# Performance work log

Hardware: AMD Instinct MI355X
Metric: run time of the kernel (lower is better)

The kernel has to match this reference:

```python
import jax, jax.numpy as jnp
import numpy as np

DIM = 64
H = 4
POS_DIM = 4
NUM_IDS = 16
B = 2048
N = 64


def setup_inputs() -> dict:
    key = jax.random.key(0)
    ks = jax.random.split(key, 16)
    d8 = DIM // 8
    stdv = 1.0 / np.sqrt(DIM * DIM)
    inp = {
        "x": jax.random.normal(ks[0], (B, N, DIM), jnp.float32),
        "pos": jax.random.normal(ks[1], (B, N, POS_DIM), jnp.float32),
        "strength": jax.random.normal(ks[2], (512,), jnp.float32),
        "embed_id1": 3,
        # weights stored [in, out] (torch Linear weight transposed)
        "Wq": jax.random.normal(ks[3], (DIM, DIM), jnp.float32) * 0.05,
        "Wk": jax.random.normal(ks[4], (DIM, DIM), jnp.float32) * 0.05,
        "pos_W1": jax.random.normal(ks[5], (POS_DIM, POS_DIM), jnp.float32) * 0.3,
        "pos_b1": jnp.zeros((POS_DIM,), jnp.float32),
        "pos_W2": jax.random.normal(ks[6], (POS_DIM, d8), jnp.float32) * 0.3,
        "pos_b2": jnp.zeros((d8,), jnp.float32),
        "head_W": jax.random.normal(ks[7], (d8, H), jnp.float32) * 0.3,
        "head_b": jnp.zeros((H,), jnp.float32),
        "gate": jnp.ones((H,), jnp.float32),
        "embeds": jax.random.uniform(ks[8], (NUM_IDS, DIM * DIM), jnp.float32, -stdv, stdv),
        "out_W": jax.random.normal(ks[9], (DIM, DIM), jnp.float32) * 0.05,
        "out_b": jnp.zeros((DIM,), jnp.float32),
        "str_W": jax.random.normal(ks[10], (512, 64), jnp.float32) * 0.04,
        "str_b": jnp.zeros((64,), jnp.float32),
    }
    return inp


def reference(x, pos, strength, embed_id1, Wq, Wk, pos_W1, pos_b1, pos_W2, pos_b2,
              head_W, head_b, gate, embeds, out_W, out_b, str_W, str_b):
    Bb, Nn, dim = x.shape
    h = gate.shape[0]
    dh = dim // h

    # strength projection, added to dynamic-weight V
    s64 = strength @ str_W + str_b                       # [dim]
    E = embeds[embed_id1].reshape(dim, dim)              # per-sample V weight
    v = x @ E.T + s64                                    # F.linear(x, E) + strength
    v = v.reshape(Bb, Nn, h, dh).transpose(0, 2, 1, 3)   # [B,H,N,dh]

    # QK attention
    q = (x @ Wq).reshape(Bb, Nn, h, dh).transpose(0, 2, 1, 3)
    k = (x @ Wk).reshape(Bb, Nn, h, dh).transpose(0, 2, 1, 3)
    attn = jax.nn.softmax(jnp.einsum('bhqd,bhkd->bhqk', q, k) / np.sqrt(dh), axis=-1)

    # pairwise relative-position attention
    p = jax.nn.relu(pos @ pos_W1 + pos_b1) @ pos_W2 + pos_b2          # [B,N,dim//8]
    diff = p[:, :, None, :] - p[:, None, :, :]                        # [B,N,N,dim//8]
    pos_logits = jnp.einsum('bqkf,fh->bhqk', diff, head_W) + head_b[None, :, None, None]
    pos_attn = jax.nn.softmax(pos_logits, axis=-1)

    # sigmoid-gated mixing + renormalization
    g = jax.nn.sigmoid(gate)[None, :, None, None]
    attn = (1.0 - g) * attn + g * pos_attn
    attn = attn / jnp.sum(attn, axis=-1, keepdims=True)

    out = jnp.einsum('bhqk,bhkd->bhqd', attn, v)
    out = out.transpose(0, 2, 1, 3).reshape(Bb, Nn, dim)
    return out @ out_W + out_b
```

## Files before the change

kernel.cpp:

```cpp
#include <hip/hip_runtime.h>

typedef unsigned short u16;
typedef unsigned int u32;
typedef short bf8 __attribute__((ext_vector_type(8)));
typedef float f4v __attribute__((ext_vector_type(4)));
typedef float f16v __attribute__((ext_vector_type(16)));

#define STR 72

__device__ __forceinline__ u32 f2bf(float f){
    union{float f;u32 i;}c; c.f=f; u32 i=c.i;
    return (i + 0x7FFFu + ((i>>16)&1u)) >> 16;
}

__device__ __forceinline__ void stage_row16(const float* __restrict__ g, short* __restrict__ dst,
                                            int n, int c0){
    const float4* p = (const float4*)(g + n*64 + c0);
    float4 a=p[0], b=p[1], c=p[2], d=p[3];
    uint4 o0, o1;
    o0.x = f2bf(a.x)|(f2bf(a.y)<<16); o0.y = f2bf(a.z)|(f2bf(a.w)<<16);
    o0.z = f2bf(b.x)|(f2bf(b.y)<<16); o0.w = f2bf(b.z)|(f2bf(b.w)<<16);
    o1.x = f2bf(c.x)|(f2bf(c.y)<<16); o1.y = f2bf(c.z)|(f2bf(c.w)<<16);
    o1.z = f2bf(d.x)|(f2bf(d.y)<<16); o1.w = f2bf(d.z)|(f2bf(d.w)<<16);
    *(uint4*)&dst[n*STR + c0]     = o0;
    *(uint4*)&dst[n*STR + c0 + 8] = o1;
}

__device__ __forceinline__ void stage_wt(const float* __restrict__ W, short* __restrict__ dst, int t){
    const int kp = t >> 3, ng = t & 7;
    const float4* r0 = (const float4*)(W + (2*kp  )*64 + 8*ng);
    const float4* r1 = (const float4*)(W + (2*kp+1)*64 + 8*ng);
    float4 a0=r0[0], a1=r0[1], b0=r1[0], b1=r1[1];
    float lo[8]={a0.x,a0.y,a0.z,a0.w,a1.x,a1.y,a1.z,a1.w};
    float hi[8]={b0.x,b0.y,b0.z,b0.w,b1.x,b1.y,b1.z,b1.w};
    #pragma unroll
    for (int i=0;i<8;++i)
        *(u32*)&dst[(8*ng+i)*STR + 2*kp] = f2bf(lo[i]) | (f2bf(hi[i])<<16);
}

__device__ __forceinline__ void mmlin(const short* __restrict__ X, const short* __restrict__ Wt,
                                      int w, int l15, int quad, f4v c[4]){
    bf8 a0 = *(const bf8*)&X[(16*w + l15)*STR + quad*8];
    bf8 a1 = *(const bf8*)&X[(16*w + l15)*STR + 32 + quad*8];
    #pragma unroll
    for (int nt=0; nt<4; ++nt){
        bf8 b0 = *(const bf8*)&Wt[(16*nt + l15)*STR + quad*8];
        bf8 b1 = *(const bf8*)&Wt[(16*nt + l15)*STR + 32 + quad*8];
        c[nt] = __builtin_amdgcn_mfma_f32_16x16x32_bf16(a0, b0, c[nt], 0,0,0);
        c[nt] = __builtin_amdgcn_mfma_f32_16x16x32_bf16(a1, b1, c[nt], 0,0,0);
    }
}

__global__ __launch_bounds__(256, 2) void attn_mfma_kernel(
    const float* __restrict__ x, const float* __restrict__ pos, const float* __restrict__ strength,
    const int* __restrict__ embed_id,
    const float* __restrict__ Wq, const float* __restrict__ Wk,
    const float* __restrict__ pW1, const float* __restrict__ pb1,
    const float* __restrict__ pW2, const float* __restrict__ pb2,
    const float* __restrict__ hW, const float* __restrict__ hb,
    const float* __restrict__ gate, const float* __restrict__ embeds,
    const float* __restrict__ oW, const float* __restrict__ ob,
    const float* __restrict__ sW, const float* __restrict__ sb,
    float* __restrict__ out)
{
    __shared__ short B0[64*STR];
    __shared__ short B1[64*STR];
    __shared__ short B2[64*STR];
    __shared__ short B3[64*STR];
    __shared__ short VT[64*STR];
    __shared__ float t_lds[4][64];
    __shared__ float sp[4][64];
    __shared__ float s64v[64];

    const int t    = threadIdx.x;
    const int b    = blockIdx.x;
    const int lane = t & 63;
    const int w    = t >> 6;
    const int l15  = lane & 15;
    const int l31  = lane & 31;
    const int l5   = lane >> 5;
    const int quad = lane >> 4;
    const int n    = t >> 2;
    const int c0   = (t & 3) << 4;

    stage_row16(x + (size_t)b*4096, B0, n, c0);
    stage_wt(Wq, B1, t);
    stage_wt(Wk, VT, t);

    {
        const int d = t & 63, part = t >> 6;
        const float* wp = sW + part*128*64 + d;
        const float* s  = strength + part*128;
        float acc = 0.f;
        #pragma unroll 8
        for (int i = 0; i < 128; ++i) acc = fmaf(s[i], wp[i*64], acc);
        sp[part][d] = acc;
    }

    if (t < 64) {
        float pv[4], h1[4], p8[8];
        const float* gp = pos + ((size_t)b*64 + t)*4;
        #pragma unroll
        for (int i = 0; i < 4; ++i) pv[i] = gp[i];
        #pragma unroll
        for (int j = 0; j < 4; ++j){
            float a = pb1[j];
            #pragma unroll
            for (int i = 0; i < 4; ++i) a = fmaf(pv[i], pW1[i*4+j], a);
            h1[j] = fmaxf(a, 0.f);
        }
        #pragma unroll
        for (int f = 0; f < 8; ++f){
            float a = pb2[f];
            #pragma unroll
            for (int j = 0; j < 4; ++j) a = fmaf(h1[j], pW2[j*8+f], a);
            p8[f] = a;
        }
        #pragma unroll
        for (int h = 0; h < 4; ++h){
            float a = 0.f;
            #pragma unroll
            for (int f = 0; f < 8; ++f) a = fmaf(p8[f], hW[f*4+h], a);
            t_lds[h][t] = a;
        }
    }
    __syncthreads();

    if (t < 64) s64v[t] = sp[0][t] + sp[1][t] + sp[2][t] + sp[3][t] + sb[t];
    {
        f4v c[4];
        #pragma unroll
        for (int nt=0;nt<4;++nt){ c[nt][0]=0.f;c[nt][1]=0.f;c[nt][2]=0.f;c[nt][3]=0.f; }
        mmlin(B0, B1, w, l15, quad, c);
        __syncthreads();
        #pragma unroll
        for (int nt=0;nt<4;++nt)
            #pragma unroll
            for (int r=0;r<4;++r)
                B2[(16*w + quad*4 + r)*STR + 16*nt + l15] = (short)f2bf(0.25f*c[nt][r]);
    }
    __syncthreads();

    {
        f4v c[4];
        #pragma unroll
        for (int nt=0;nt<4;++nt){ c[nt][0]=0.f;c[nt][1]=0.f;c[nt][2]=0.f;c[nt][3]=0.f; }
        mmlin(B0, VT, w, l15, quad, c);
        stage_row16(embeds + (size_t)(*embed_id)*4096, B1, n, c0);
        __syncthreads();
        #pragma unroll
        for (int nt=0;nt<4;++nt)
            #pragma unroll
            for (int r=0;r<4;++r)
                B3[(16*w + quad*4 + r)*STR + 16*nt + l15] = (short)f2bf(c[nt][r]);
    }
    __syncthreads();

    {
        f4v c[4];
        #pragma unroll
        for (int nt=0;nt<4;++nt){ c[nt][0]=0.f;c[nt][1]=0.f;c[nt][2]=0.f;c[nt][3]=0.f; }
        mmlin(B0, B1, w, l15, quad, c);
        #pragma unroll
        for (int nt=0;nt<4;++nt){
            float sv = s64v[16*nt + l15];
            uint2 pk;
            pk.x = f2bf(c[nt][0]+sv) | (f2bf(c[nt][1]+sv)<<16);
            pk.y = f2bf(c[nt][2]+sv) | (f2bf(c[nt][3]+sv)<<16);
            *(uint2*)&VT[(16*nt + l15)*STR + 16*w + quad*4] = pk;
        }
    }
    __syncthreads();

    float g = 1.f/(1.f + __expf(-gate[w]));
    f16v S[2][2];
    {
        bf8 ka0 = *(const bf8*)&B3[(     l31)*STR + 16*w + 8*l5];
        bf8 ka1 = *(const bf8*)&B3[(32 + l31)*STR + 16*w + 8*l5];
        bf8 qb0 = *(const bf8*)&B2[(     l31)*STR + 16*w + 8*l5];
        bf8 qb1 = *(const bf8*)&B2[(32 + l31)*STR + 16*w + 8*l5];
        #pragma unroll
        for (int mt=0;mt<2;++mt)
            #pragma unroll
            for (int nt=0;nt<2;++nt)
                #pragma unroll
                for (int i=0;i<16;++i) S[mt][nt][i] = 0.f;
        S[0][0] = __builtin_amdgcn_mfma_f32_32x32x16_bf16(ka0, qb0, S[0][0], 0,0,0);
        S[0][1] = __builtin_amdgcn_mfma_f32_32x32x16_bf16(ka0, qb1, S[0][1], 0,0,0);
        S[1][0] = __builtin_amdgcn_mfma_f32_32x32x16_bf16(ka1, qb0, S[1][0], 0,0,0);
        S[1][1] = __builtin_amdgcn_mfma_f32_32x32x16_bf16(ka1, qb1, S[1][1], 0,0,0);
    }
    float ep[32];
    {
        #pragma unroll
        for (int mt=0;mt<2;++mt)
            #pragma unroll
            for (int rg=0;rg<4;++rg){
                float4 tv = *(const float4*)&t_lds[w][32*mt + 8*rg + 4*l5];
                ep[mt*16+rg*4+0] = -tv.x; ep[mt*16+rg*4+1] = -tv.y;
                ep[mt*16+rg*4+2] = -tv.z; ep[mt*16+rg*4+3] = -tv.w;
            }
        float mx = ep[0];
        #pragma unroll
        for (int i=1;i<32;++i) mx = fmaxf(mx, ep[i]);
        mx = fmaxf(mx, __shfl_xor(mx, 32));
        float sm = 0.f;
        #pragma unroll
        for (int i=0;i<32;++i){ ep[i] = __expf(ep[i]-mx); sm += ep[i]; }
        sm += __shfl_xor(sm, 32);
        float gi = g / sm;
        #pragma unroll
        for (int i=0;i<32;++i) ep[i] *= gi;
    }
    float inv[2];
    #pragma unroll
    for (int nt=0;nt<2;++nt){
        float m = S[0][nt][0];
        #pragma unroll
        for (int i=1;i<16;++i) m = fmaxf(m, S[0][nt][i]);
        #pragma unroll
        for (int i=0;i<16;++i) m = fmaxf(m, S[1][nt][i]);
        m = fmaxf(m, __shfl_xor(m, 32));
        float l = 0.f;
        #pragma unroll
        for (int mt=0;mt<2;++mt)
            #pragma unroll
            for (int i=0;i<16;++i){ float e = __expf(S[mt][nt][i]-m); S[mt][nt][i] = e; l += e; }
        l += __shfl_xor(l, 32);
        float c1 = (1.f - g) / l;
        float tot = 0.f;
        #pragma unroll
        for (int mt=0;mt<2;++mt)
            #pragma unroll
            for (int i=0;i<16;++i){ float a = fmaf(c1, S[mt][nt][i], ep[mt*16+i]); S[mt][nt][i] = a; tot += a; }
        tot += __shfl_xor(tot, 32);
        inv[nt] = 1.f / tot;
    }
    __syncthreads();

    short* Pb = (w==0) ? B0 : (w==1) ? B1 : (w==2) ? B2 : B3;
    #pragma unroll
    for (int nt=0;nt<2;++nt)
        #pragma unroll
        for (int mt=0;mt<2;++mt)
            #pragma unroll
            for (int rg=0;rg<4;++rg){
                float v0 = S[mt][nt][rg*4+0]*inv[nt], v1 = S[mt][nt][rg*4+1]*inv[nt];
                float v2 = S[mt][nt][rg*4+2]*inv[nt], v3 = S[mt][nt][rg*4+3]*inv[nt];
                uint2 pk;
                pk.x = f2bf(v0) | (f2bf(v1)<<16);
                pk.y = f2bf(v2) | (f2bf(v3)<<16);
                *(uint2*)&Pb[(32*nt + l31)*STR + 32*mt + 8*rg + 4*l5] = pk;
            }

    f4v o[4];
    {
        bf8 bv0 = *(const bf8*)&VT[(16*w + l15)*STR + quad*8];
        bf8 bv1 = *(const bf8*)&VT[(16*w + l15)*STR + 32 + quad*8];
        #pragma unroll
        for (int mt=0;mt<4;++mt){
            o[mt][0]=0.f;o[mt][1]=0.f;o[mt][2]=0.f;o[mt][3]=0.f;
            bf8 a0 = *(const bf8*)&Pb[(16*mt + l15)*STR + quad*8];
            bf8 a1 = *(const bf8*)&Pb[(16*mt + l15)*STR + 32 + quad*8];
            o[mt] = __builtin_amdgcn_mfma_f32_16x16x32_bf16(a0, bv0, o[mt], 0,0,0);
            o[mt] = __builtin_amdgcn_mfma_f32_16x16x32_bf16(a1, bv1, o[mt], 0,0,0);
        }
    }
    __syncthreads();

    #pragma unroll
    for (int mt=0;mt<4;++mt)
        #pragma unroll
        for (int r=0;r<4;++r)
            B3[(16*mt + quad*4 + r)*STR + 16*w + l15] = (short)f2bf(o[mt][r]);
    stage_wt(oW, B1, t);
    __syncthreads();

    {
        f4v c[4];
        #pragma unroll
        for (int nt=0;nt<4;++nt){
            float obv = ob[16*nt + l15];
            c[nt][0]=obv;c[nt][1]=obv;c[nt][2]=obv;c[nt][3]=obv;
        }
        mmlin(B3, B1, w, l15, quad, c);
        #pragma unroll
        for (int nt=0;nt<4;++nt)
            #pragma unroll
            for (int r=0;r<4;++r)
                out[((size_t)b*64 + 16*w + quad*4 + r)*64 + 16*nt + l15] = c[nt][r];
    }
}

extern "C" void kernel_launch(void* const* d_in, const int* in_sizes, int n_in,
                              void* d_out, int out_size, void* d_ws, size_t ws_size,
                              hipStream_t stream) {
    const int B = in_sizes[0] / (64 * 64);
    attn_mfma_kernel<<<B, 256, 0, stream>>>(
        (const float*)d_in[0],  (const float*)d_in[1],  (const float*)d_in[2],  (const int*)d_in[3],
        (const float*)d_in[4],  (const float*)d_in[5],  (const float*)d_in[6],  (const float*)d_in[7],
        (const float*)d_in[8],  (const float*)d_in[9],  (const float*)d_in[10], (const float*)d_in[11],
        (const float*)d_in[12], (const float*)d_in[13], (const float*)d_in[14], (const float*)d_in[15],
        (const float*)d_in[16], (const float*)d_in[17], (float*)d_out);
}
```

Baseline: 149.1 us.

## Split per-batch invariant weight prep into a pre-kernel and merge Q/K projections

Adds a pre-kernel that converts Wq, Wk, out_W and the selected embed matrix to bf16 once, computes the strength projection once, and precomputes each batch's position-attention softmax into workspace. The main kernel then copies pre-converted bf16 tiles instead of redoing the conversion and strength matvec in every block. It also issues the Q and K matmuls back to back and drops a barrier, using an extra LDS buffer (PX). The cost is a second kernel launch, more workspace traffic and more LDS per block, which may lower occupancy.

```diff
diff --git a/kernel.cpp b/kernel.cpp
--- a/kernel.cpp
+++ b/kernel.cpp
@@ -26,16 +26,12 @@
     *(uint4*)&dst[n*STR + c0 + 8] = o1;
 }
 
-__device__ __forceinline__ void stage_wt(const float* __restrict__ W, short* __restrict__ dst, int t){
-    const int kp = t >> 3, ng = t & 7;
-    const float4* r0 = (const float4*)(W + (2*kp  )*64 + 8*ng);
-    const float4* r1 = (const float4*)(W + (2*kp+1)*64 + 8*ng);
-    float4 a0=r0[0], a1=r0[1], b0=r1[0], b1=r1[1];
-    float lo[8]={a0.x,a0.y,a0.z,a0.w,a1.x,a1.y,a1.z,a1.w};
-    float hi[8]={b0.x,b0.y,b0.z,b0.w,b1.x,b1.y,b1.z,b1.w};
-    #pragma unroll
-    for (int i=0;i<8;++i)
-        *(u32*)&dst[(8*ng+i)*STR + 2*kp] = f2bf(lo[i]) | (f2bf(hi[i])<<16);
+__device__ __forceinline__ void copy8k(const u16* __restrict__ src, short* __restrict__ dst, int t){
+    const int r = t >> 2, cs = (t & 3) << 4;
+    const uint4* s = (const uint4*)(src + r*64 + cs);
+    uint4 a = s[0], b = s[1];
+    *(uint4*)&dst[r*STR + cs]     = a;
+    *(uint4*)&dst[r*STR + cs + 8] = b;
 }
 
 __device__ __forceinline__ void mmlin(const short* __restrict__ X, const short* __restrict__ Wt,
@@ -51,16 +47,111 @@
     }
 }
 
-__global__ __launch_bounds__(256, 2) void attn_mfma_kernel(
-    const float* __restrict__ x, const float* __restrict__ pos, const float* __restrict__ strength,
+__global__ __launch_bounds__(256) void pre_kernel(
+    const float* __restrict__ pos, const float* __restrict__ strength,
     const int* __restrict__ embed_id,
     const float* __restrict__ Wq, const float* __restrict__ Wk,
     const float* __restrict__ pW1, const float* __restrict__ pb1,
     const float* __restrict__ pW2, const float* __restrict__ pb2,
-    const float* __restrict__ hW, const float* __restrict__ hb,
-    const float* __restrict__ gate, const float* __restrict__ embeds,
-    const float* __restrict__ oW, const float* __restrict__ ob,
-    const float* __restrict__ sW, const float* __restrict__ sb,
+    const float* __restrict__ hW, const float* __restrict__ embeds,
+    const float* __restrict__ oW, const float* __restrict__ sW,
+    const float* __restrict__ sb,
+    float* __restrict__ ws_s64, float* __restrict__ ws_pat,
+    u16* __restrict__ ws_wq, u16* __restrict__ ws_wk,
+    u16* __restrict__ ws_ow, u16* __restrict__ ws_e, int B)
+{
+    const int blk = blockIdx.x;
+    const int t = threadIdx.x;
+
+    if (blk < B) {
+        __shared__ float t_l[4][64];
+        if (t < 64) {
+            float pv[4], h1[4], p8[8];
+            const float* gp = pos + ((size_t)blk*64 + t)*4;
+            #pragma unroll
+            for (int i = 0; i < 4; ++i) pv[i] = gp[i];
+            #pragma unroll
+            for (int j = 0; j < 4; ++j){
+                float a = pb1[j];
+                #pragma unroll
+                for (int i = 0; i < 4; ++i) a = fmaf(pv[i], pW1[i*4+j], a);
+                h1[j] = fmaxf(a, 0.f);
+            }
+            #pragma unroll
+            for (int f = 0; f < 8; ++f){
+                float a = pb2[f];
+                #pragma unroll
+                for (int j = 0; j < 4; ++j) a = fmaf(h1[j], pW2[j*8+f], a);
+                p8[f] = a;
+            }
+            #pragma unroll
+            for (int h = 0; h < 4; ++h){
+                float a = 0.f;
+                #pragma unroll
+                for (int f = 0; f < 8; ++f) a = fmaf(p8[f], hW[f*4+h], a);
+                t_l[h][t] = a;
+            }
+        }
+        __syncthreads();
+        const int h = t >> 6, k = t & 63;
+        float v0 = -t_l[h][k];
+        float m = v0;
+        #pragma unroll
+        for (int off = 32; off; off >>= 1) m = fmaxf(m, __shfl_xor(m, off));
+        float e = __expf(v0 - m);
+        float ssum = e;
+        #pragma unroll
+        for (int off = 32; off; off >>= 1) ssum += __shfl_xor(ssum, off);
+        ws_pat[((size_t)blk*4 + h)*64 + k] = e / ssum;
+        return;
+    }
+
+    const int j = blk - B;
+    if (j < 3) {
+        const float* W = (j==0) ? Wq : (j==1) ? Wk : oW;
+        u16* dst = (j==0) ? ws_wq : (j==1) ? ws_wk : ws_ow;
+        const int kp = t >> 3, ng = t & 7;
+        const float4* r0 = (const float4*)(W + (2*kp  )*64 + 8*ng);
+        const float4* r1 = (const float4*)(W + (2*kp+1)*64 + 8*ng);
+        float4 a0=r0[0], a1=r0[1], b0=r1[0], b1=r1[1];
+        float lo[8]={a0.x,a0.y,a0.z,a0.w,a1.x,a1.y,a1.z,a1.w};
+        float hi[8]={b0.x,b0.y,b0.z,b0.w,b1.x,b1.y,b1.z,b1.w};
+        #pragma unroll
+        for (int i=0;i<8;++i)
+            *(u32*)&dst[(8*ng+i)*64 + 2*kp] = f2bf(lo[i]) | (f2bf(hi[i])<<16);
+    } else {
+        __shared__ float sp[4][64];
+        {
+            const int n = t >> 2, c0 = (t & 3) << 4;
+            const float4* p = (const float4*)(embeds + (size_t)(*embed_id)*4096 + n*64 + c0);
+            float4 a=p[0], b=p[1], c=p[2], d=p[3];
+            uint4 o0, o1;
+            o0.x = f2bf(a.x)|(f2bf(a.y)<<16); o0.y = f2bf(a.z)|(f2bf(a.w)<<16);
+            o0.z = f2bf(b.x)|(f2bf(b.y)<<16); o0.w = f2bf(b.z)|(f2bf(b.w)<<16);
+            o1.x = f2bf(c.x)|(f2bf(c.y)<<16); o1.y = f2bf(c.z)|(f2bf(c.w)<<16);
+            o1.z = f2bf(d.x)|(f2bf(d.y)<<16); o1.w = f2bf(d.z)|(f2bf(d.w)<<16);
+            *(uint4*)&ws_e[n*64 + c0]     = o0;
+            *(uint4*)&ws_e[n*64 + c0 + 8] = o1;
+        }
+        {
+            const int d = t & 63, part = t >> 6;
+            const float* wp = sW + part*128*64 + d;
+            const float* s  = strength + part*128;
+            float acc = 0.f;
+            #pragma unroll 8
+            for (int i = 0; i < 128; ++i) acc = fmaf(s[i], wp[i*64], acc);
+            sp[part][d] = acc;
+        }
+        __syncthreads();
+        if (t < 64) ws_s64[t] = sp[0][t] + sp[1][t] + sp[2][t] + sp[3][t] + sb[t];
+    }
+}
+
+__global__ __launch_bounds__(256, 2) void attn_main_kernel(
+    const float* __restrict__ x, const float* __restrict__ gate, const float* __restrict__ ob,
+    const float* __restrict__ ws_s64, const float* __restrict__ ws_pat,
+    const u16* __restrict__ ws_wq, const u16* __restrict__ ws_wk,
+    const u16* __restrict__ ws_ow, const u16* __restrict__ ws_e,
     float* __restrict__ out)
 {
     __shared__ short B0[64*STR];
@@ -68,9 +159,7 @@
     __shared__ short B2[64*STR];
     __shared__ short B3[64*STR];
     __shared__ short VT[64*STR];
-    __shared__ float t_lds[4][64];
-    __shared__ float sp[4][64];
-    __shared__ float s64v[64];
+    __shared__ short PX[64*STR];
 
     const int t    = threadIdx.x;
     const int b    = blockIdx.x;
@@ -84,49 +173,49 @@
     const int c0   = (t & 3) << 4;
 
     stage_row16(x + (size_t)b*4096, B0, n, c0);
-    stage_wt(Wq, B1, t);
-    stage_wt(Wk, VT, t);
-
-    {
-        const int d = t & 63, part = t >> 6;
-        const float* wp = sW + part*128*64 + d;
-        const float* s  = strength + part*128;
-        float acc = 0.f;
-        #pragma unroll 8
-        for (int i = 0; i < 128; ++i) acc = fmaf(s[i], wp[i*64], acc);
-        sp[part][d] = acc;
-    }
-
-    if (t < 64) {
-        float pv[4], h1[4], p8[8];
-        const float* gp = pos + ((size_t)b*64 + t)*4;
-        #pragma unroll
-        for (int i = 0; i < 4; ++i) pv[i] = gp[i];
-        #pragma unroll
-        for (int j = 0; j < 4; ++j){
-            float a = pb1[j];
-            #pragma unroll
-            for (int i = 0; i < 4; ++i) a = fmaf(pv[i], pW1[i*4+j], a);
-            h1[j] = fmaxf(a, 0.f);
-        }
-        #pragma unroll
-        for (int f = 0; f < 8; ++f){
-            float a = pb2[f];
-            #pragma unroll
-            for (int j = 0; j < 4; ++j) a = fmaf(h1[j], pW2[j*8+f], a);
-            p8[f] = a;
-        }
-        #pragma unroll
-        for (int h = 0; h < 4; ++h){
-            float a = 0.f;
-            #pragma unroll
-            for (int f = 0; f < 8; ++f) a = fmaf(p8[f], hW[f*4+h], a);
-            t_lds[h][t] = a;
-        }
-    }
-    __syncthreads();
-
-    if (t < 64) s64v[t] = sp[0][t] + sp[1][t] + sp[2][t] + sp[3][t] + sb[t];
+    copy8k(ws_wq, B1, t);
+    copy8k(ws_wk, VT, t);
+
+    uint4 eA, eB, owA, owB;
+    {
+        const int r = t >> 2, cs = (t & 3) << 4;
+        const uint4* se = (const uint4*)(ws_e + r*64 + cs);
+        eA = se[0]; eB = se[1];
+        const uint4* so = (const uint4*)(ws_ow + r*64 + cs);
+        owA = so[0]; owB = so[1];
+    }
+    float svv[4];
+    #pragma unroll
+    for (int nt=0;nt<4;++nt) svv[nt] = ws_s64[16*nt + l15];
+    float g = 1.f/(1.f + __expf(-gate[w]));
+    float obv[4];
+    #pragma unroll
+    for (int nt=0;nt<4;++nt) obv[nt] = ob[16*nt + l15];
+    __syncthreads();
+
+    {
+        f4v cq[4], ck[4];
+        #pragma unroll
+        for (int nt=0;nt<4;++nt){
+            cq[nt][0]=0.f;cq[nt][1]=0.f;cq[nt][2]=0.f;cq[nt][3]=0.f;
+            ck[nt][0]=0.f;ck[nt][1]=0.f;ck[nt][2]=0.f;ck[nt][3]=0.f;
+        }
+        mmlin(B0, B1, w, l15, quad, cq);
+        mmlin(B0, VT, w, l15, quad, ck);
+        __syncthreads();
+        #pragma unroll
+        for (int nt=0;nt<4;++nt)
+            #pragma unroll
+            for (int r=0;r<4;++r){
+                B2[(16*w + quad*4 + r)*STR + 16*nt + l15] = (short)f2bf(0.25f*cq[nt][r]);
+                B3[(16*w + quad*4 + r)*STR + 16*nt + l15] = (short)f2bf(ck[nt][r]);
+            }
+        const int r = t >> 2, cs = (t & 3) << 4;
+        *(uint4*)&B1[r*STR + cs]     = eA;
+        *(uint4*)&B1[r*STR + cs + 8] = eB;
+    }
+    __syncthreads();
+
     {
         f4v c[4];
         #pragma unroll
@@ -134,45 +223,19 @@
         mmlin(B0, B1, w, l15, quad, c);
         __syncthreads();
         #pragma unroll
-        for (int nt=0;nt<4;++nt)
-            #pragma unroll
-            for (int r=0;r<4;++r)
-                B2[(16*w + quad*4 + r)*STR + 16*nt + l15] = (short)f2bf(0.25f*c[nt][r]);
-    }
-    __syncthreads();
-
-    {
-        f4v c[4];
-        #pragma unroll
-        for (int nt=0;nt<4;++nt){ c[nt][0]=0.f;c[nt][1]=0.f;c[nt][2]=0.f;c[nt][3]=0.f; }
-        mmlin(B0, VT, w, l15, quad, c);
-        stage_row16(embeds + (size_t)(*embed_id)*4096, B1, n, c0);
-        __syncthreads();
-        #pragma unroll
-        for (int nt=0;nt<4;++nt)
-            #pragma unroll
-            for (int r=0;r<4;++r)
-                B3[(16*w + quad*4 + r)*STR + 16*nt + l15] = (short)f2bf(c[nt][r]);
-    }
-    __syncthreads();
-
-    {
-        f4v c[4];
-        #pragma unroll
-        for (int nt=0;nt<4;++nt){ c[nt][0]=0.f;c[nt][1]=0.f;c[nt][2]=0.f;c[nt][3]=0.f; }
-        mmlin(B0, B1, w, l15, quad, c);
-        #pragma unroll
         for (int nt=0;nt<4;++nt){
-            float sv = s64v[16*nt + l15];
+            float sv = svv[nt];
             uint2 pk;
             pk.x = f2bf(c[nt][0]+sv) | (f2bf(c[nt][1]+sv)<<16);
             pk.y = f2bf(c[nt][2]+sv) | (f2bf(c[nt][3]+sv)<<16);
             *(uint2*)&VT[(16*nt + l15)*STR + 16*w + quad*4] = pk;
         }
-    }
-    __syncthreads();
-
-    float g = 1.f/(1.f + __expf(-gate[w]));
+        const int r = t >> 2, cs = (t & 3) << 4;
+        *(uint4*)&B1[r*STR + cs]     = owA;
+        *(uint4*)&B1[r*STR + cs + 8] = owB;
+    }
+    __syncthreads();
+
     f16v S[2][2];
     {
         bf8 ka0 = *(const bf8*)&B3[(     l31)*STR + 16*w + 8*l5];
@@ -192,25 +255,15 @@
     }
     float ep[32];
     {
+        const float* pp = ws_pat + ((size_t)b*4 + w)*64;
         #pragma unroll
         for (int mt=0;mt<2;++mt)
             #pragma unroll
             for (int rg=0;rg<4;++rg){
-                float4 tv = *(const float4*)&t_lds[w][32*mt + 8*rg + 4*l5];
-                ep[mt*16+rg*4+0] = -tv.x; ep[mt*16+rg*4+1] = -tv.y;
-                ep[mt*16+rg*4+2] = -tv.z; ep[mt*16+rg*4+3] = -tv.w;
-            }
-        float mx = ep[0];
-        #pragma unroll
-        for (int i=1;i<32;++i) mx = fmaxf(mx, ep[i]);
-        mx = fmaxf(mx, __shfl_xor(mx, 32));
-        float sm = 0.f;
-        #pragma unroll
-        for (int i=0;i<32;++i){ ep[i] = __expf(ep[i]-mx); sm += ep[i]; }
-        sm += __shfl_xor(sm, 32);
-        float gi = g / sm;
-        #pragma unroll
-        for (int i=0;i<32;++i) ep[i] *= gi;
+                float4 tv = *(const float4*)&pp[32*mt + 8*rg + 4*l5];
+                ep[mt*16+rg*4+0] = g*tv.x; ep[mt*16+rg*4+1] = g*tv.y;
+                ep[mt*16+rg*4+2] = g*tv.z; ep[mt*16+rg*4+3] = g*tv.w;
+            }
     }
     float inv[2];
     #pragma unroll
@@ -238,7 +291,7 @@
     }
     __syncthreads();
 
-    short* Pb = (w==0) ? B0 : (w==1) ? B1 : (w==2) ? B2 : B3;
+    short* Pb = (w==0) ? B0 : (w==1) ? PX : (w==2) ? B2 : B3;
     #pragma unroll
     for (int nt=0;nt<2;++nt)
         #pragma unroll
@@ -273,15 +326,13 @@
         #pragma unroll
         for (int r=0;r<4;++r)
             B3[(16*mt + quad*4 + r)*STR + 16*w + l15] = (short)f2bf(o[mt][r]);
-    stage_wt(oW, B1, t);
     __syncthreads();
 
     {
         f4v c[4];
         #pragma unroll
         for (int nt=0;nt<4;++nt){
-            float obv = ob[16*nt + l15];
-            c[nt][0]=obv;c[nt][1]=obv;c[nt][2]=obv;c[nt][3]=obv;
+            c[nt][0]=obv[nt];c[nt][1]=obv[nt];c[nt][2]=obv[nt];c[nt][3]=obv[nt];
         }
         mmlin(B3, B1, w, l15, quad, c);
         #pragma unroll
@@ -296,10 +347,24 @@
                               void* d_out, int out_size, void* d_ws, size_t ws_size,
                               hipStream_t stream) {
     const int B = in_sizes[0] / (64 * 64);
-    attn_mfma_kernel<<<B, 256, 0, stream>>>(
-        (const float*)d_in[0],  (const float*)d_in[1],  (const float*)d_in[2],  (const int*)d_in[3],
-        (const float*)d_in[4],  (const float*)d_in[5],  (const float*)d_in[6],  (const float*)d_in[7],
-        (const float*)d_in[8],  (const float*)d_in[9],  (const float*)d_in[10], (const float*)d_in[11],
-        (const float*)d_in[12], (const float*)d_in[13], (const float*)d_in[14], (const float*)d_in[15],
-        (const float*)d_in[16], (const float*)d_in[17], (float*)d_out);
-}
+
+    float* ws_s64 = (float*)d_ws;
+    float* ws_pat = ws_s64 + 64;
+    u16*   ws_wq  = (u16*)(ws_pat + (size_t)B*4*64);
+    u16*   ws_wk  = ws_wq + 4096;
+    u16*   ws_ow  = ws_wk + 4096;
+    u16*   ws_e   = ws_ow + 4096;
+
+    pre_kernel<<<B + 4, 256, 0, stream>>>(
+        (const float*)d_in[1],  (const float*)d_in[2],  (const int*)d_in[3],
+        (const float*)d_in[4],  (const float*)d_in[5],
+        (const float*)d_in[6],  (const float*)d_in[7],  (const float*)d_in[8],  (const float*)d_in[9],
+        (const float*)d_in[10], (const float*)d_in[13], (const float*)d_in[14],
+        (const float*)d_in[16], (const float*)d_in[17],
+        ws_s64, ws_pat, ws_wq, ws_wk, ws_ow, ws_e, B);
+
+    attn_main_kernel<<<B, 256, 0, stream>>>(
+        (const float*)d_in[0],  (const float*)d_in[12], (const float*)d_in[15],
+        ws_s64, ws_pat, ws_wq, ws_wk, ws_ow, ws_e,
+        (float*)d_out);
+}
```

New measurement: 140.4 us. 5.9% less time.
